# Kernel optimization log

Hardware: AMD Instinct MI355X
Metric: run time of the kernel (lower is better)

The kernel has to match this reference:

```python
import jax, jax.numpy as jnp
import numpy as np

ATT_DEPTH = 3
PATCH = 8


def setup_inputs() -> dict:
    key = jax.random.key(0)
    k1, k2 = jax.random.split(key)
    B, C, H, W = 8, 16, 512, 512
    x = jax.random.normal(k1, (B, C, H, W), dtype=jnp.float32)
    L = (H // PATCH) * (W // PATCH)            # 4096 target patches
    Lp = (H // (PATCH * 2 ** ATT_DEPTH)) * (W // (PATCH * 2 ** ATT_DEPTH))  # 64 source patches
    attentions = jax.random.uniform(k2, (B, 1, L, Lp), dtype=jnp.float32)
    return {"x": x, "attentions": attentions}


def reference(x, attentions):
    B, C, H, W = x.shape
    d = 2 ** ATT_DEPTH
    p = PATCH
    # depthwise ones-conv stride d, divided by d*d == average pooling
    argx = x.reshape(B, C, H // d, d, W // d, d).mean(axis=(3, 5))  # [B,C,h,w]
    h, w = H // d, W // d
    hp, wp = h // p, w // p
    # nn.Unfold(kernel=p, stride=p): channels ordered (C, kh, kw), locations row-major
    unf = (argx.reshape(B, C, hp, p, wp, p)
               .transpose(0, 1, 3, 5, 2, 4)
               .reshape(B, C * p * p, hp * wp))  # [B, C*p*p, L']
    # normalize attention rows by nonzero count (non-differentiable int count)
    nz = jax.lax.stop_gradient(
        jnp.count_nonzero(attentions, axis=-1).astype(attentions.dtype)
    )[..., None] + 1e-05  # [B,1,L,1]
    # [B,1,L,L'] @ [B,1,L',C*p*p] -> [B,1,L,C*p*p]
    att = jnp.matmul(attentions / nz, unf[:, None].transpose(0, 1, 3, 2))
    att = jnp.squeeze(att, axis=1).transpose(0, 2, 1)  # [B, C*p*p, L]
    # Fold(output=(H,W), kernel=p, stride=p): non-overlapping -> pure reshape
    Hp, Wp = H // p, W // p
    out = (att.reshape(B, C, p, p, Hp, Wp)
              .transpose(0, 1, 4, 2, 5, 3)
              .reshape(B, C, H, W))
    return out
```

## Files before the change

kernel.cpp:

```cpp
#include <hip/hip_runtime.h>
#include <hip/hip_bf16.h>

typedef __attribute__((ext_vector_type(4))) float f32x4;
typedef __attribute__((ext_vector_type(8))) short s16x8;

#define NB 8
#define NC 16
#define HH 512
#define WW 512

__global__ __launch_bounds__(256) void pool_to_bt(const float* __restrict__ x,
                                                  __hip_bfloat16* __restrict__ bt) {
    int flat = blockIdx.x * 256 + threadIdx.x;
    int wq = flat & 63;
    int hq = (flat >> 6) & 63;
    int c  = (flat >> 12) & 15;
    int b  = flat >> 16;
    const float* base = x + ((size_t)(b * NC + c) * HH + hq * 8) * WW + wq * 8;
    float s = 0.f;
#pragma unroll
    for (int r = 0; r < 8; ++r) {
        f32x4 v0 = *(const f32x4*)(base + (size_t)r * WW);
        f32x4 v1 = *(const f32x4*)(base + (size_t)r * WW + 4);
        s += v0[0] + v0[1] + v0[2] + v0[3] + v1[0] + v1[1] + v1[2] + v1[3];
    }
    s *= (1.f / 64.f);
    int m  = c * 64 + (hq & 7) * 8 + (wq & 7);
    int lp = (hq >> 3) * 8 + (wq >> 3);
    bt[((size_t)b * 1024 + m) * 64 + lp] = __float2bfloat16(s);
}

__global__ __launch_bounds__(256, 5) void gemm_scatter(const float* __restrict__ attn,
                                                       const __hip_bfloat16* __restrict__ bt,
                                                       float* __restrict__ out) {
    int mb = blockIdx.x;
    int lb = blockIdx.y;
    int b  = blockIdx.z;

    __shared__ __align__(16) unsigned short As[128][64];
    __shared__ __align__(16) unsigned short Bs[128][64];

    int tid = threadIdx.x;

    {
        const unsigned short* Bg = (const unsigned short*)bt + ((size_t)b * 1024 + mb * 128) * 64;
#pragma unroll
        for (int i = 0; i < 4; ++i) {
            int cid = tid + i * 256;
            int row = cid >> 3, p = cid & 7;
            const unsigned short* gsrc = Bg + row * 64 + (p ^ (row & 7)) * 8;
            __builtin_amdgcn_global_load_lds(
                (const __attribute__((address_space(1))) void*)gsrc,
                (__attribute__((address_space(3))) void*)(&Bs[0][0] + (size_t)cid * 8),
                16, 0, 0);
        }
    }
    {
        int row  = tid >> 1;
        int half = tid & 1;
        const float* Arow = attn + ((size_t)(b * 4096 + lb * 128 + row)) * 64 + half * 32;
        f32x4 v[8];
        int cnt = 0;
#pragma unroll
        for (int j = 0; j < 8; ++j) {
            v[j] = *(const f32x4*)(Arow + j * 4);
            cnt += (v[j][0] != 0.f) + (v[j][1] != 0.f) + (v[j][2] != 0.f) + (v[j][3] != 0.f);
        }
        cnt += __shfl_xor(cnt, 1);
        float inv = 1.0f / ((float)cnt + 1e-5f);
#pragma unroll
        for (int j = 0; j < 4; ++j) {
            s16x8 o;
#pragma unroll
            for (int e = 0; e < 8; ++e) {
                __hip_bfloat16 h = __float2bfloat16(v[j * 2 + (e >> 2)][e & 3] * inv);
                o[e] = (short)*reinterpret_cast<unsigned short*>(&h);
            }
            int p = (half * 4 + j) ^ (row & 7);
            *(s16x8*)&As[row][p * 8] = o;
        }
    }
    __syncthreads();

    int w    = tid >> 6;
    int lane = tid & 63;
    int wm   = (w & 1) * 64;
    int wl   = (w >> 1) * 64;
    int lr   = lane & 15;
    int kq   = lane >> 4;
    int sw   = lr & 7;

    f32x4 acc[4][4] = {};
#pragma unroll
    for (int ks = 0; ks < 2; ++ks) {
        int p = (ks * 4 + kq) ^ sw;
        s16x8 mf[4], lf[4];
#pragma unroll
        for (int i = 0; i < 4; ++i)
            mf[i] = *(const s16x8*)&Bs[wm + i * 16 + lr][p * 8];
#pragma unroll
        for (int j = 0; j < 4; ++j)
            lf[j] = *(const s16x8*)&As[wl + j * 16 + lr][p * 8];
#pragma unroll
        for (int i = 0; i < 4; ++i)
#pragma unroll
            for (int j = 0; j < 4; ++j)
                acc[i][j] = __builtin_amdgcn_mfma_f32_16x16x32_bf16(mf[i], lf[j], acc[i][j], 0, 0, 0);
    }

#pragma unroll
    for (int mi = 0; mi < 4; ++mi) {
        int m0 = mb * 128 + wm + mi * 16 + kq * 4;
        int c  = m0 >> 6, kh = (m0 >> 3) & 7, kw = m0 & 7;
        float* obase = out + (((size_t)(b * NC + c) * HH) + kh) * WW + kw;
#pragma unroll
        for (int lj = 0; lj < 4; ++lj) {
            int l  = lb * 128 + wl + lj * 16 + lr;
            int Hp = l >> 6, Wp = l & 63;
            *(f32x4*)(obase + ((size_t)Hp * 8) * WW + Wp * 8) = acc[mi][lj];
        }
    }
}

extern "C" void kernel_launch(void* const* d_in, const int* in_sizes, int n_in,
                              void* d_out, int out_size, void* d_ws, size_t ws_size,
                              hipStream_t stream) {
    const float* x    = (const float*)d_in[0];
    const float* attn = (const float*)d_in[1];
    float* out        = (float*)d_out;

    __hip_bfloat16* bt = (__hip_bfloat16*)d_ws;

    pool_to_bt<<<2048, 256, 0, stream>>>(x, bt);
    dim3 grid(8, 32, 8);
    gemm_scatter<<<grid, 256, 0, stream>>>(attn, bt, out);
}
```

Baseline: 56.20 us.

## Precompute normalized bf16 attention in prep kernel and load it via global_load_lds

Moves the attention nonzero-count normalization and bf16 conversion out of the GEMM blocks into the pooling prep kernel, writing a bf16 copy to workspace. The GEMM then loads both operands with direct global-to-LDS loads. This removes the per-block redundant fp32 reads and VALU conversion that were repeated across the 8 M-blocks. In exchange it adds an extra 4 MB write and read through workspace.

Result: faster. 54.58 us (-2.9%).

```diff
diff --git a/kernel.cpp b/kernel.cpp
--- a/kernel.cpp
+++ b/kernel.cpp
@@ -2,6 +2,7 @@
 #include <hip/hip_bf16.h>
 
 typedef __attribute__((ext_vector_type(4))) float f32x4;
+typedef __attribute__((ext_vector_type(4))) short s16x4;
 typedef __attribute__((ext_vector_type(8))) short s16x8;
 
 #define NB 8
@@ -9,28 +10,50 @@
 #define HH 512
 #define WW 512
 
-__global__ __launch_bounds__(256) void pool_to_bt(const float* __restrict__ x,
-                                                  __hip_bfloat16* __restrict__ bt) {
+__global__ __launch_bounds__(256) void prep(const float* __restrict__ x,
+                                            const float* __restrict__ attn,
+                                            __hip_bfloat16* __restrict__ bt,
+                                            __hip_bfloat16* __restrict__ abf) {
     int flat = blockIdx.x * 256 + threadIdx.x;
-    int wq = flat & 63;
-    int hq = (flat >> 6) & 63;
-    int c  = (flat >> 12) & 15;
-    int b  = flat >> 16;
-    const float* base = x + ((size_t)(b * NC + c) * HH + hq * 8) * WW + wq * 8;
-    float s = 0.f;
+    {
+        int wq = flat & 63;
+        int hq = (flat >> 6) & 63;
+        int c  = (flat >> 12) & 15;
+        int b  = flat >> 16;
+        const float* base = x + ((size_t)(b * NC + c) * HH + hq * 8) * WW + wq * 8;
+        float s = 0.f;
 #pragma unroll
-    for (int r = 0; r < 8; ++r) {
-        f32x4 v0 = *(const f32x4*)(base + (size_t)r * WW);
-        f32x4 v1 = *(const f32x4*)(base + (size_t)r * WW + 4);
-        s += v0[0] + v0[1] + v0[2] + v0[3] + v1[0] + v1[1] + v1[2] + v1[3];
+        for (int r = 0; r < 8; ++r) {
+            f32x4 v0 = *(const f32x4*)(base + (size_t)r * WW);
+            f32x4 v1 = *(const f32x4*)(base + (size_t)r * WW + 4);
+            s += v0[0] + v0[1] + v0[2] + v0[3] + v1[0] + v1[1] + v1[2] + v1[3];
+        }
+        s *= (1.f / 64.f);
+        int m  = c * 64 + (hq & 7) * 8 + (wq & 7);
+        int lp = (hq >> 3) * 8 + (wq >> 3);
+        bt[((size_t)b * 1024 + m) * 64 + lp] = __float2bfloat16(s);
     }
-    s *= (1.f / 64.f);
-    int m  = c * 64 + (hq & 7) * 8 + (wq & 7);
-    int lp = (hq >> 3) * 8 + (wq >> 3);
-    bt[((size_t)b * 1024 + m) * 64 + lp] = __float2bfloat16(s);
+    {
+        int row   = flat >> 4;
+        int chunk = flat & 15;
+        f32x4 v = *(const f32x4*)(attn + (size_t)row * 64 + chunk * 4);
+        int cnt = (v[0] != 0.f) + (v[1] != 0.f) + (v[2] != 0.f) + (v[3] != 0.f);
+        cnt += __shfl_xor(cnt, 1);
+        cnt += __shfl_xor(cnt, 2);
+        cnt += __shfl_xor(cnt, 4);
+        cnt += __shfl_xor(cnt, 8);
+        float inv = 1.0f / ((float)cnt + 1e-5f);
+        s16x4 o;
+#pragma unroll
+        for (int e = 0; e < 4; ++e) {
+            __hip_bfloat16 h = __float2bfloat16(v[e] * inv);
+            o[e] = (short)*reinterpret_cast<unsigned short*>(&h);
+        }
+        *(s16x4*)((unsigned short*)abf + (size_t)row * 64 + chunk * 4) = o;
+    }
 }
 
-__global__ __launch_bounds__(256, 5) void gemm_scatter(const float* __restrict__ attn,
+__global__ __launch_bounds__(256, 5) void gemm_scatter(const __hip_bfloat16* __restrict__ abf,
                                                        const __hip_bfloat16* __restrict__ bt,
                                                        float* __restrict__ out) {
     int mb = blockIdx.x;
@@ -43,41 +66,21 @@
     int tid = threadIdx.x;
 
     {
-        const unsigned short* Bg = (const unsigned short*)bt + ((size_t)b * 1024 + mb * 128) * 64;
+        const unsigned short* Ag = (const unsigned short*)abf + ((size_t)b * 4096 + lb * 128) * 64;
+        const unsigned short* Bg = (const unsigned short*)bt  + ((size_t)b * 1024 + mb * 128) * 64;
 #pragma unroll
         for (int i = 0; i < 4; ++i) {
             int cid = tid + i * 256;
             int row = cid >> 3, p = cid & 7;
-            const unsigned short* gsrc = Bg + row * 64 + (p ^ (row & 7)) * 8;
+            int src = row * 64 + (p ^ (row & 7)) * 8;
             __builtin_amdgcn_global_load_lds(
-                (const __attribute__((address_space(1))) void*)gsrc,
+                (const __attribute__((address_space(1))) void*)(Ag + src),
+                (__attribute__((address_space(3))) void*)(&As[0][0] + (size_t)cid * 8),
+                16, 0, 0);
+            __builtin_amdgcn_global_load_lds(
+                (const __attribute__((address_space(1))) void*)(Bg + src),
                 (__attribute__((address_space(3))) void*)(&Bs[0][0] + (size_t)cid * 8),
                 16, 0, 0);
-        }
-    }
-    {
-        int row  = tid >> 1;
-        int half = tid & 1;
-        const float* Arow = attn + ((size_t)(b * 4096 + lb * 128 + row)) * 64 + half * 32;
-        f32x4 v[8];
-        int cnt = 0;
-#pragma unroll
-        for (int j = 0; j < 8; ++j) {
-            v[j] = *(const f32x4*)(Arow + j * 4);
-            cnt += (v[j][0] != 0.f) + (v[j][1] != 0.f) + (v[j][2] != 0.f) + (v[j][3] != 0.f);
-        }
-        cnt += __shfl_xor(cnt, 1);
-        float inv = 1.0f / ((float)cnt + 1e-5f);
-#pragma unroll
-        for (int j = 0; j < 4; ++j) {
-            s16x8 o;
-#pragma unroll
-            for (int e = 0; e < 8; ++e) {
-                __hip_bfloat16 h = __float2bfloat16(v[j * 2 + (e >> 2)][e & 3] * inv);
-                o[e] = (short)*reinterpret_cast<unsigned short*>(&h);
-            }
-            int p = (half * 4 + j) ^ (row & 7);
-            *(s16x8*)&As[row][p * 8] = o;
         }
     }
     __syncthreads();
@@ -129,9 +132,10 @@
     const float* attn = (const float*)d_in[1];
     float* out        = (float*)d_out;
 
-    __hip_bfloat16* bt = (__hip_bfloat16*)d_ws;
+    __hip_bfloat16* bt  = (__hip_bfloat16*)d_ws;
+    __hip_bfloat16* abf = (__hip_bfloat16*)((char*)d_ws + (1 << 20));
 
-    pool_to_bt<<<2048, 256, 0, stream>>>(x, bt);
+    prep<<<2048, 256, 0, stream>>>(x, attn, bt, abf);
     dim3 grid(8, 32, 8);
-    gemm_scatter<<<grid, 256, 0, stream>>>(attn, bt, out);
+    gemm_scatter<<<grid, 256, 0, stream>>>(abf, bt, out);
 }
```
